# Kernel tuning notes

Hardware: AMD Instinct MI355X
Metric: run time of the kernel (lower is better)

The kernel has to match this reference:

```python
import jax, jax.numpy as jnp
import numpy as np

NUM_HEADS = 8
SR_RATIO = 2
LN_EPS = 1e-5


def setup_inputs() -> dict:
    key = jax.random.key(0)
    ks = jax.random.split(key, 8)
    B, N, C = 8, 4096, 512
    s = 0.02  # weight init scale to keep logits sane
    return {
        "x": jax.random.normal(ks[0], (B, N, C), jnp.float32),
        "q_w": jax.random.normal(ks[1], (C, C), jnp.float32) * s,
        "q_b": jnp.zeros((C,), jnp.float32),
        "kv_w": jax.random.normal(ks[2], (2 * C, C), jnp.float32) * s,
        "kv_b": jnp.zeros((2 * C,), jnp.float32),
        "sr_w": jax.random.normal(ks[3], (C, C, SR_RATIO, SR_RATIO), jnp.float32) * s,
        "sr_b": jnp.zeros((C,), jnp.float32),
        "ln_g": jnp.ones((C,), jnp.float32),
        "ln_b": jnp.zeros((C,), jnp.float32),
        "proj_w": jax.random.normal(ks[4], (C, C), jnp.float32) * s,
        "proj_b": jnp.zeros((C,), jnp.float32),
        "H": 64,
        "W": 64,
    }


def _layernorm(x, g, b):
    mu = jnp.mean(x, axis=-1, keepdims=True)
    var = jnp.var(x, axis=-1, keepdims=True)
    return (x - mu) * jax.lax.rsqrt(var + LN_EPS) * g + b


def reference(x, q_w, q_b, kv_w, kv_b, sr_w, sr_b, ln_g, ln_b, proj_w, proj_b, H, W):
    B, N, C = x.shape
    h = NUM_HEADS
    d = C // h
    scale = d ** (-0.5)

    # q: [B, h, N, d]
    q = (x @ q_w.T + q_b).reshape(B, N, h, d).transpose(0, 2, 1, 3)

    # spatial reduction: Conv2d(C, C, k=SR, stride=SR) on [B, C, H, W]
    x_img = x.transpose(0, 2, 1).reshape(B, C, H, W)
    x_sr = jax.lax.conv_general_dilated(
        x_img, sr_w,
        window_strides=(SR_RATIO, SR_RATIO), padding="VALID",
        dimension_numbers=("NCHW", "OIHW", "NCHW"),
    ) + sr_b[None, :, None, None]
    N2 = (H // SR_RATIO) * (W // SR_RATIO)
    x_sr = x_sr.reshape(B, C, N2).transpose(0, 2, 1)  # [B, N2, C]
    x_sr = _layernorm(x_sr, ln_g, ln_b)

    # kv: [2, B, h, N2, d]
    kv = (x_sr @ kv_w.T + kv_b).reshape(B, N2, 2, h, d).transpose(2, 0, 3, 1, 4)
    k, v = kv[0], kv[1]

    attn = jax.nn.softmax(jnp.einsum("bhnd,bhmd->bhnm", q, k) * scale, axis=-1)
    out = jnp.einsum("bhnm,bhmd->bhnd", attn, v)  # [B, h, N, d]
    out = out.transpose(0, 2, 1, 3).reshape(B, N, C)
    return out @ proj_w.T + proj_b
```

## Files before the change

kernel.cpp:

```cpp
#include <hip/hip_runtime.h>
#include <hip/hip_bf16.h>

typedef __hip_bfloat16 bf16;
typedef __bf16 bf16x8 __attribute__((ext_vector_type(8)));
typedef float f32x16 __attribute__((ext_vector_type(16)));
typedef unsigned int u32;
typedef unsigned int u32x2 __attribute__((ext_vector_type(2)));

typedef const __attribute__((address_space(1))) void GV;
typedef __attribute__((address_space(3))) void LV;

#define TM 128
#define TN 128
#define TK 64

static __device__ __forceinline__ float fexp2(float x) {
#if __has_builtin(__builtin_amdgcn_exp2f)
    return __builtin_amdgcn_exp2f(x);
#else
    return exp2f(x);
#endif
}

__global__ void prep_k(const float* __restrict__ x, const float* __restrict__ qw,
                       const float* __restrict__ kvw, const float* __restrict__ pjw,
                       const float* __restrict__ srw,
                       bf16* __restrict__ xb, bf16* __restrict__ qwb,
                       bf16* __restrict__ kvwb, bf16* __restrict__ pjwb,
                       bf16* __restrict__ srwb) {
    const int bid = blockIdx.x;
    const int tid = threadIdx.x;
    if (bid < 17408) {
        const float* src;
        bf16* dst;
        int i;
        if (bid < 16384)      { src = x;   dst = xb;   i = bid * 256 + tid; }
        else if (bid < 16640) { src = qw;  dst = qwb;  i = (bid - 16384) * 256 + tid; }
        else if (bid < 17152) { src = kvw; dst = kvwb; i = (bid - 16640) * 256 + tid; }
        else                  { src = pjw; dst = pjwb; i = (bid - 17152) * 256 + tid; }
        float4 a = reinterpret_cast<const float4*>(src)[i];
        bf16* d = dst + (size_t)i * 4;
        d[0] = __float2bfloat16(a.x);
        d[1] = __float2bfloat16(a.y);
        d[2] = __float2bfloat16(a.z);
        d[3] = __float2bfloat16(a.w);
    } else {
        int idx = (bid - 17408) * 256 + tid;
        int co = idx >> 11;
        int t  = idx & 2047;
        int p  = t >> 9;
        int ci = t & 511;
        srwb[idx] = __float2bfloat16(srw[(size_t)co * 2048 + ci * 4 + p]);
    }
}

template<int KIND>
__device__ __forceinline__ void gemm_body(int bid, bf16* ldsA, bf16* ldsB,
                                          const bf16* __restrict__ A, const bf16* __restrict__ Bw,
                                          const float* __restrict__ bias,
                                          bf16* __restrict__ outB, bf16* __restrict__ outB2,
                                          float* __restrict__ outF, int N, int K) {
    const int tid = threadIdx.x;
    const int lane = tid & 63;
    const int wave = tid >> 6;
    const int ntn = N / TN;
    const int row0 = (bid / ntn) * TM;
    const int col0 = (bid % ntn) * TN;
    const int wm = wave >> 1, wn = wave & 1;
    const int l31 = lane & 31;
    const int hi8 = lane >> 5;
    const int NK = K / TK;

    f32x16 acc[2][2];
#pragma unroll
    for (int i = 0; i < 2; ++i)
#pragma unroll
        for (int j = 0; j < 2; ++j) acc[i][j] = f32x16{};

    auto stage = [&](int ks, int buf) {
        const int k0 = ks * TK;
        bf16* la = ldsA + buf * (TM * TK);
        bf16* lb = ldsB + buf * (TM * TK);
#pragma unroll
        for (int t = 0; t < 4; ++t) {
            int idx = t * 256 + tid;
            int r = idx >> 3;
            int c = ((idx & 7) ^ (r & 7)) * 8;
            const bf16* src;
            if (KIND == 1) {
                int rr = row0 + r;
                int k = k0 + c;
                int p = k >> 9, ci = k & 511;
                int b = rr >> 10, ii = (rr >> 5) & 31, jj = rr & 31;
                int n_in = (2 * ii + (p >> 1)) * 64 + 2 * jj + (p & 1);
                src = A + ((size_t)(b * 4096 + n_in)) * 512 + ci;
            } else {
                src = A + (size_t)(row0 + r) * K + k0 + c;
            }
            __builtin_amdgcn_global_load_lds((GV*)src, (LV*)&la[idx * 8], 16, 0, 0);
        }
#pragma unroll
        for (int t = 0; t < 4; ++t) {
            int idx = t * 256 + tid;
            int r = idx >> 3;
            int c = ((idx & 7) ^ (r & 7)) * 8;
            const bf16* src = Bw + (size_t)(col0 + r) * K + k0 + c;
            __builtin_amdgcn_global_load_lds((GV*)src, (LV*)&lb[idx * 8], 16, 0, 0);
        }
    };

    stage(0, 0);
    stage(1, 1);

    int cur = 0;
    for (int ks = 0; ks < NK; ++ks) {
        if (ks < NK - 1) asm volatile("s_waitcnt vmcnt(8)" ::: "memory");
        else             asm volatile("s_waitcnt vmcnt(0)" ::: "memory");
        __builtin_amdgcn_s_barrier();

        const bf16* la = ldsA + cur * (TM * TK);
        const bf16* lb = ldsB + cur * (TM * TK);
#pragma unroll
        for (int kk = 0; kk < 4; ++kk) {
            bf16x8 af[2], bfr[2];
#pragma unroll
            for (int m = 0; m < 2; ++m) {
                int row = wm * 64 + m * 32 + l31;
                int chunk = (kk * 2 + hi8) ^ (row & 7);
                af[m] = *reinterpret_cast<const bf16x8*>(&la[row * 64 + chunk * 8]);
            }
#pragma unroll
            for (int n = 0; n < 2; ++n) {
                int row = wn * 64 + n * 32 + l31;
                int chunk = (kk * 2 + hi8) ^ (row & 7);
                bfr[n] = *reinterpret_cast<const bf16x8*>(&lb[row * 64 + chunk * 8]);
            }
#pragma unroll
            for (int m = 0; m < 2; ++m)
#pragma unroll
                for (int n = 0; n < 2; ++n)
                    acc[m][n] = __builtin_amdgcn_mfma_f32_32x32x16_bf16(af[m], bfr[n], acc[m][n], 0, 0, 0);
        }

        __builtin_amdgcn_s_barrier();
        if (ks + 2 < NK) stage(ks + 2, cur);
        cur ^= 1;
    }

#pragma unroll
    for (int m = 0; m < 2; ++m) {
#pragma unroll
        for (int n = 0; n < 2; ++n) {
#pragma unroll
            for (int r = 0; r < 16; ++r) {
                int grow = row0 + wm * 64 + m * 32 + (r & 3) + 8 * (r >> 2) + 4 * (lane >> 5);
                int gcol = col0 + wn * 64 + n * 32 + l31;
                float v = acc[m][n][r] + bias[gcol];
                if (KIND == 0) {
                    int b = grow >> 12, nn = grow & 4095;
                    int h = gcol >> 6, dd = gcol & 63;
                    outB[(((size_t)(b * 8 + h)) * 4096 + nn) * 64 + dd] =
                        __float2bfloat16(v * 0.18033688011112042f);
                } else if (KIND == 1) {
                    outF[(size_t)grow * 512 + gcol] = v;
                } else if (KIND == 2) {
                    int b = grow >> 10, mm = grow & 1023;
                    if (gcol < 512) {
                        int h = gcol >> 6, dd = gcol & 63;
                        outB[(((size_t)(b * 8 + h)) * 1024 + mm) * 64 + dd] = __float2bfloat16(v);
                    } else {
                        int c2 = gcol - 512;
                        int h = c2 >> 6, dd = c2 & 63;
                        outB2[(((size_t)(b * 8 + h)) * 64 + dd) * 1024 + mm] = __float2bfloat16(v);
                    }
                } else {
                    outF[(size_t)grow * 512 + gcol] = v;
                }
            }
        }
    }
}

__launch_bounds__(256, 2)
__global__ void gemm01_k(const bf16* __restrict__ xb, const bf16* __restrict__ qw,
                         const bf16* __restrict__ srw, const float* __restrict__ q_b,
                         const float* __restrict__ sr_b,
                         bf16* __restrict__ q_out, float* __restrict__ xsr_out) {
    __shared__ __align__(16) bf16 ldsA[2][TM * TK];
    __shared__ __align__(16) bf16 ldsB[2][TM * TK];
    if (blockIdx.x < 256)
        gemm_body<1>(blockIdx.x, &ldsA[0][0], &ldsB[0][0], xb, srw, sr_b,
                     nullptr, nullptr, xsr_out, 512, 2048);
    else
        gemm_body<0>(blockIdx.x - 256, &ldsA[0][0], &ldsB[0][0], xb, qw, q_b,
                     q_out, nullptr, nullptr, 512, 512);
}

__launch_bounds__(256, 2)
__global__ void gemm2_k(const bf16* __restrict__ A, const bf16* __restrict__ Bw,
                        const float* __restrict__ bias,
                        bf16* __restrict__ kout, bf16* __restrict__ vtout) {
    __shared__ __align__(16) bf16 ldsA[2][TM * TK];
    __shared__ __align__(16) bf16 ldsB[2][TM * TK];
    gemm_body<2>(blockIdx.x, &ldsA[0][0], &ldsB[0][0], A, Bw, bias, kout, vtout, nullptr, 1024, 512);
}

__launch_bounds__(256, 2)
__global__ void gemm3_k(const bf16* __restrict__ A, const bf16* __restrict__ Bw,
                        const float* __restrict__ bias, float* __restrict__ outF) {
    __shared__ __align__(16) bf16 ldsA[2][TM * TK];
    __shared__ __align__(16) bf16 ldsB[2][TM * TK];
    gemm_body<3>(blockIdx.x, &ldsA[0][0], &ldsB[0][0], A, Bw, bias, nullptr, nullptr, outF, 512, 512);
}

__global__ void ln_k(const float* __restrict__ xsr, const float* __restrict__ g,
                     const float* __restrict__ bta, bf16* __restrict__ out) {
    const int row = blockIdx.x;
    const int tid = threadIdx.x;
    const float* xr = xsr + (size_t)row * 512;
    float2 v = *reinterpret_cast<const float2*>(xr + tid * 2);
    float s = v.x + v.y;
    float sq = v.x * v.x + v.y * v.y;
#pragma unroll
    for (int m = 1; m < 64; m <<= 1) {
        s += __shfl_xor(s, m, 64);
        sq += __shfl_xor(sq, m, 64);
    }
    __shared__ float rs[4], rq[4];
    int wave = tid >> 6, lane = tid & 63;
    if (lane == 0) { rs[wave] = s; rq[wave] = sq; }
    __syncthreads();
    s = rs[0] + rs[1] + rs[2] + rs[3];
    sq = rq[0] + rq[1] + rq[2] + rq[3];
    float mu = s * (1.f / 512.f);
    float var = sq * (1.f / 512.f) - mu * mu;
    float rstd = rsqrtf(var + 1e-5f);
    bf16* orow = out + (size_t)row * 512;
    orow[tid * 2]     = __float2bfloat16((v.x - mu) * rstd * g[tid * 2] + bta[tid * 2]);
    orow[tid * 2 + 1] = __float2bfloat16((v.y - mu) * rstd * g[tid * 2 + 1] + bta[tid * 2 + 1]);
}

__launch_bounds__(256, 4)
__global__ void attn_k(const bf16* __restrict__ Q, const bf16* __restrict__ Kb,
                       const bf16* __restrict__ Vt, bf16* __restrict__ Out) {
    const int p = blockIdx.x;
    const int bh = (p & 7) * 8 + (p >> 8);
    const int qb = (p >> 3) & 31;
    const int b = bh >> 3, h = bh & 7;
    const int tid = threadIdx.x, lane = tid & 63, wave = tid >> 6;
    const int q0 = qb * 128 + wave * 32;
    const int l31 = lane & 31;
    const int klo8 = (lane >> 5) * 8;

    const bf16* Qp = Q + ((size_t)bh * 4096 + q0) * 64;
    const bf16* Kp = Kb + (size_t)bh * 1024 * 64;
    const bf16* Vp = Vt + (size_t)bh * 64 * 1024;

    __shared__ __align__(16) char smem[32768];

    bf16x8 qf[4];
#pragma unroll
    for (int c = 0; c < 4; ++c)
        qf[c] = *reinterpret_cast<const bf16x8*>(Qp + (size_t)l31 * 64 + c * 16 + klo8);

    f32x16 accO[2];
    accO[0] = f32x16{};
    accO[1] = f32x16{};
    f32x16 accL = f32x16{};
    const f32x16 z16 = f32x16{};

    union { u32 u[4]; bf16x8 v; } onesu;
    onesu.u[0] = 0x3F803F80u; onesu.u[1] = 0x3F803F80u;
    onesu.u[2] = 0x3F803F80u; onesu.u[3] = 0x3F803F80u;
    const bf16x8 ones8 = onesu.v;

    const int l2 = lane >> 1;
    const int lh8 = (lane & 1) * 8;
    const int w16 = wave * 16;

    const char* rb = smem + l31 * 32 + (lane >> 5) * 16;

#define STAGE_TILE(KT, BASE)                                                              \
    do {                                                                                  \
        char* _b = (BASE);                                                                \
        __builtin_amdgcn_global_load_lds((GV*)(Kp + (size_t)((KT) + l2) * 64 + w16 + lh8),\
                                         (LV*)(_b + wave * 2048), 16, 0, 0);              \
        __builtin_amdgcn_global_load_lds((GV*)(Kp + (size_t)((KT) + 32 + l2) * 64 + w16 + lh8),\
                                         (LV*)(_b + wave * 2048 + 1024), 16, 0, 0);       \
        __builtin_amdgcn_global_load_lds((GV*)(Vp + (size_t)l2 * 1024 + (KT) + w16 + lh8),\
                                         (LV*)(_b + 8192 + wave * 2048), 16, 0, 0);       \
        __builtin_amdgcn_global_load_lds((GV*)(Vp + (size_t)(32 + l2) * 1024 + (KT) + w16 + lh8),\
                                         (LV*)(_b + 8192 + wave * 2048 + 1024), 16, 0, 0);\
    } while (0)

    STAGE_TILE(0, smem);
    STAGE_TILE(64, smem + 16384);

    int cur = 0;
    for (int t = 0; t < 16; ++t) {
        if (t < 15) asm volatile("s_waitcnt vmcnt(4)" ::: "memory");
        else        asm volatile("s_waitcnt vmcnt(0)" ::: "memory");
        __builtin_amdgcn_s_barrier();

        const char* rc = rb + cur * 16384;

        bf16x8 kf0[4], kf1[4];
#pragma unroll
        for (int c = 0; c < 4; ++c) {
            kf0[c] = *reinterpret_cast<const bf16x8*>(rc + c * 2048);
            kf1[c] = *reinterpret_cast<const bf16x8*>(rc + c * 2048 + 1024);
        }
        f32x16 sA = __builtin_amdgcn_mfma_f32_32x32x16_bf16(kf0[0], qf[0], z16, 0, 0, 0);
        f32x16 sB = __builtin_amdgcn_mfma_f32_32x32x16_bf16(kf1[0], qf[0], z16, 0, 0, 0);
#pragma unroll
        for (int c = 1; c < 4; ++c) {
            sA = __builtin_amdgcn_mfma_f32_32x32x16_bf16(kf0[c], qf[c], sA, 0, 0, 0);
            sB = __builtin_amdgcn_mfma_f32_32x32x16_bf16(kf1[c], qf[c], sB, 0, 0, 0);
        }

        float pA[16], pB[16];
#pragma unroll
        for (int r = 0; r < 16; ++r) pA[r] = fexp2(sA[r]);
#pragma unroll
        for (int r = 0; r < 16; ++r) pB[r] = fexp2(sB[r]);

        u32 wA[8], wB[8];
#pragma unroll
        for (int k = 0; k < 8; ++k) {
            union { __hip_bfloat162 h2; u32 u; } cv;
            cv.h2 = __float22bfloat162_rn(float2{pA[2 * k], pA[2 * k + 1]});
            wA[k] = cv.u;
            union { __hip_bfloat162 h2; u32 u; } cw;
            cw.h2 = __float22bfloat162_rn(float2{pB[2 * k], pB[2 * k + 1]});
            wB[k] = cw.u;
        }
        union { u32 u[4]; bf16x8 v; } fr[4];
        {
            u32x2 e0 = __builtin_amdgcn_permlane32_swap(wA[0], wA[2], false, false);
            u32x2 e1 = __builtin_amdgcn_permlane32_swap(wA[1], wA[3], false, false);
            fr[0].u[0] = e0[0]; fr[0].u[1] = e1[0]; fr[0].u[2] = e0[1]; fr[0].u[3] = e1[1];
            u32x2 e2 = __builtin_amdgcn_permlane32_swap(wA[4], wA[6], false, false);
            u32x2 e3 = __builtin_amdgcn_permlane32_swap(wA[5], wA[7], false, false);
            fr[1].u[0] = e2[0]; fr[1].u[1] = e3[0]; fr[1].u[2] = e2[1]; fr[1].u[3] = e3[1];
            u32x2 e4 = __builtin_amdgcn_permlane32_swap(wB[0], wB[2], false, false);
            u32x2 e5 = __builtin_amdgcn_permlane32_swap(wB[1], wB[3], false, false);
            fr[2].u[0] = e4[0]; fr[2].u[1] = e5[0]; fr[2].u[2] = e4[1]; fr[2].u[3] = e5[1];
            u32x2 e6 = __builtin_amdgcn_permlane32_swap(wB[4], wB[6], false, false);
            u32x2 e7 = __builtin_amdgcn_permlane32_swap(wB[5], wB[7], false, false);
            fr[3].u[0] = e6[0]; fr[3].u[1] = e7[0]; fr[3].u[2] = e6[1]; fr[3].u[3] = e7[1];
        }

        __builtin_amdgcn_s_setprio(1);
#pragma unroll
        for (int dd = 0; dd < 2; ++dd) {
#pragma unroll
            for (int kk = 0; kk < 4; ++kk) {
                bf16x8 vv = *reinterpret_cast<const bf16x8*>(rc + 8192 + kk * 2048 + dd * 1024);
                accO[dd] = __builtin_amdgcn_mfma_f32_32x32x16_bf16(vv, fr[kk].v, accO[dd], 0, 0, 0);
            }
        }
#pragma unroll
        for (int kk = 0; kk < 4; ++kk)
            accL = __builtin_amdgcn_mfma_f32_32x32x16_bf16(ones8, fr[kk].v, accL, 0, 0, 0);
        __builtin_amdgcn_s_setprio(0);

        __builtin_amdgcn_s_barrier();
        if (t + 2 < 16) STAGE_TILE((t + 2) * 64, smem + cur * 16384);
        cur ^= 1;
    }

    __syncthreads();

    typedef bf16 (*ObufT)[32][72];
    ObufT obuf = (ObufT)smem;
    float inv = 1.f / accL[0];
#pragma unroll
    for (int dd = 0; dd < 2; ++dd)
#pragma unroll
        for (int r = 0; r < 16; r += 2) {
            int d = dd * 32 + (r & 3) + 8 * (r >> 2) + 4 * (lane >> 5);
            union { __hip_bfloat162 h2; u32 u; } cv;
            cv.h2 = __float22bfloat162_rn(float2{accO[dd][r] * inv, accO[dd][r + 1] * inv});
            *reinterpret_cast<u32*>(&obuf[wave][l31][d]) = cv.u;
        }
    __syncthreads();
    {
        int qr = lane >> 1, hf = lane & 1;
        const bf16* orow = &obuf[wave][qr][hf * 32];
        bf16* gout = Out + ((size_t)b * 4096 + q0 + qr) * 512 + h * 64 + hf * 32;
#pragma unroll
        for (int j = 0; j < 4; ++j) {
            bf16x8 t2 = *reinterpret_cast<const bf16x8*>(orow + j * 8);
            *reinterpret_cast<bf16x8*>(gout + j * 8) = t2;
        }
    }
#undef STAGE_TILE
}

extern "C" void kernel_launch(void* const* d_in, const int* in_sizes, int n_in,
                              void* d_out, int out_size, void* d_ws, size_t ws_size,
                              hipStream_t stream) {
    const float* x      = (const float*)d_in[0];
    const float* q_w    = (const float*)d_in[1];
    const float* q_b    = (const float*)d_in[2];
    const float* kv_w   = (const float*)d_in[3];
    const float* kv_b   = (const float*)d_in[4];
    const float* sr_w   = (const float*)d_in[5];
    const float* sr_b   = (const float*)d_in[6];
    const float* ln_g   = (const float*)d_in[7];
    const float* ln_b   = (const float*)d_in[8];
    const float* proj_w = (const float*)d_in[9];
    const float* proj_b = (const float*)d_in[10];

    char* w = (char*)d_ws;
    bf16* x_bf   = (bf16*)w; w += (size_t)8 * 4096 * 512 * 2;
    bf16* q_bf   = (bf16*)w; w += (size_t)8 * 4096 * 512 * 2;
    bf16* qw_bf  = (bf16*)w; w += (size_t)512 * 512 * 2;
    bf16* kvw_bf = (bf16*)w; w += (size_t)1024 * 512 * 2;
    bf16* srw_bf = (bf16*)w; w += (size_t)512 * 2048 * 2;
    bf16* pjw_bf = (bf16*)w; w += (size_t)512 * 512 * 2;
    float* xsr_f = (float*)w; w += (size_t)8 * 1024 * 512 * 4;
    bf16* xsrb   = (bf16*)w; w += (size_t)8 * 1024 * 512 * 2;
    bf16* k_bf   = (bf16*)w; w += (size_t)8 * 8 * 1024 * 64 * 2;
    bf16* vt_bf  = (bf16*)w; w += (size_t)8 * 8 * 1024 * 64 * 2;
    bf16* ao_bf  = (bf16*)w; w += (size_t)8 * 4096 * 512 * 2;

    prep_k<<<dim3(21504), dim3(256), 0, stream>>>(x, q_w, kv_w, proj_w, sr_w,
                                                  x_bf, qw_bf, kvw_bf, pjw_bf, srw_bf);

    gemm01_k<<<dim3(1280), dim3(256), 0, stream>>>(x_bf, qw_bf, srw_bf, q_b, sr_b, q_bf, xsr_f);
    ln_k<<<dim3(8192), dim3(256), 0, stream>>>(xsr_f, ln_g, ln_b, xsrb);
    gemm2_k<<<dim3(512), dim3(256), 0, stream>>>(xsrb, kvw_bf, kv_b, k_bf, vt_bf);
    attn_k<<<dim3(2048), dim3(256), 0, stream>>>(q_bf, k_bf, vt_bf, ao_bf);
    gemm3_k<<<dim3(1024), dim3(256), 0, stream>>>(ao_bf, pjw_bf, proj_b, (float*)d_out);
}
```

Measured before the change: 235.3 us.

## Replace double-buffered GEMM LDS pipeline with single buffer for higher occupancy

Measured after the change: 234.9 us. Within noise of the previous version (-0.1%).

```diff
diff --git a/kernel.cpp b/kernel.cpp
--- a/kernel.cpp
+++ b/kernel.cpp
@@ -77,10 +77,8 @@
 #pragma unroll
         for (int j = 0; j < 2; ++j) acc[i][j] = f32x16{};
 
-    auto stage = [&](int ks, int buf) {
+    for (int ks = 0; ks < NK; ++ks) {
         const int k0 = ks * TK;
-        bf16* la = ldsA + buf * (TM * TK);
-        bf16* lb = ldsB + buf * (TM * TK);
 #pragma unroll
         for (int t = 0; t < 4; ++t) {
             int idx = t * 256 + tid;
@@ -97,7 +95,7 @@
             } else {
                 src = A + (size_t)(row0 + r) * K + k0 + c;
             }
-            __builtin_amdgcn_global_load_lds((GV*)src, (LV*)&la[idx * 8], 16, 0, 0);
+            __builtin_amdgcn_global_load_lds((GV*)src, (LV*)&ldsA[idx * 8], 16, 0, 0);
         }
 #pragma unroll
         for (int t = 0; t < 4; ++t) {
@@ -105,21 +103,10 @@
             int r = idx >> 3;
             int c = ((idx & 7) ^ (r & 7)) * 8;
             const bf16* src = Bw + (size_t)(col0 + r) * K + k0 + c;
-            __builtin_amdgcn_global_load_lds((GV*)src, (LV*)&lb[idx * 8], 16, 0, 0);
-        }
-    };
-
-    stage(0, 0);
-    stage(1, 1);
-
-    int cur = 0;
-    for (int ks = 0; ks < NK; ++ks) {
-        if (ks < NK - 1) asm volatile("s_waitcnt vmcnt(8)" ::: "memory");
-        else             asm volatile("s_waitcnt vmcnt(0)" ::: "memory");
-        __builtin_amdgcn_s_barrier();
-
-        const bf16* la = ldsA + cur * (TM * TK);
-        const bf16* lb = ldsB + cur * (TM * TK);
+            __builtin_amdgcn_global_load_lds((GV*)src, (LV*)&ldsB[idx * 8], 16, 0, 0);
+        }
+        __syncthreads();
+
 #pragma unroll
         for (int kk = 0; kk < 4; ++kk) {
             bf16x8 af[2], bfr[2];
@@ -127,13 +114,13 @@
             for (int m = 0; m < 2; ++m) {
                 int row = wm * 64 + m * 32 + l31;
                 int chunk = (kk * 2 + hi8) ^ (row & 7);
-                af[m] = *reinterpret_cast<const bf16x8*>(&la[row * 64 + chunk * 8]);
+                af[m] = *reinterpret_cast<const bf16x8*>(&ldsA[row * 64 + chunk * 8]);
             }
 #pragma unroll
             for (int n = 0; n < 2; ++n) {
                 int row = wn * 64 + n * 32 + l31;
                 int chunk = (kk * 2 + hi8) ^ (row & 7);
-                bfr[n] = *reinterpret_cast<const bf16x8*>(&lb[row * 64 + chunk * 8]);
+                bfr[n] = *reinterpret_cast<const bf16x8*>(&ldsB[row * 64 + chunk * 8]);
             }
 #pragma unroll
             for (int m = 0; m < 2; ++m)
@@ -141,10 +128,7 @@
                 for (int n = 0; n < 2; ++n)
                     acc[m][n] = __builtin_amdgcn_mfma_f32_32x32x16_bf16(af[m], bfr[n], acc[m][n], 0, 0, 0);
         }
-
-        __builtin_amdgcn_s_barrier();
-        if (ks + 2 < NK) stage(ks + 2, cur);
-        cur ^= 1;
+        __syncthreads();
     }
 
 #pragma unroll
@@ -181,36 +165,36 @@
     }
 }
 
-__launch_bounds__(256, 2)
+__launch_bounds__(256, 3)
 __global__ void gemm01_k(const bf16* __restrict__ xb, const bf16* __restrict__ qw,
                          const bf16* __restrict__ srw, const float* __restrict__ q_b,
                          const float* __restrict__ sr_b,
                          bf16* __restrict__ q_out, float* __restrict__ xsr_out) {
-    __shared__ __align__(16) bf16 ldsA[2][TM * TK];
-    __shared__ __align__(16) bf16 ldsB[2][TM * TK];
+    __shared__ __align__(16) bf16 ldsA[TM * TK];
+    __shared__ __align__(16) bf16 ldsB[TM * TK];
     if (blockIdx.x < 256)
-        gemm_body<1>(blockIdx.x, &ldsA[0][0], &ldsB[0][0], xb, srw, sr_b,
+        gemm_body<1>(blockIdx.x, ldsA, ldsB, xb, srw, sr_b,
                      nullptr, nullptr, xsr_out, 512, 2048);
     else
-        gemm_body<0>(blockIdx.x - 256, &ldsA[0][0], &ldsB[0][0], xb, qw, q_b,
+        gemm_body<0>(blockIdx.x - 256, ldsA, ldsB, xb, qw, q_b,
                      q_out, nullptr, nullptr, 512, 512);
 }
 
-__launch_bounds__(256, 2)
+__launch_bounds__(256, 3)
 __global__ void gemm2_k(const bf16* __restrict__ A, const bf16* __restrict__ Bw,
                         const float* __restrict__ bias,
                         bf16* __restrict__ kout, bf16* __restrict__ vtout) {
-    __shared__ __align__(16) bf16 ldsA[2][TM * TK];
-    __shared__ __align__(16) bf16 ldsB[2][TM * TK];
-    gemm_body<2>(blockIdx.x, &ldsA[0][0], &ldsB[0][0], A, Bw, bias, kout, vtout, nullptr, 1024, 512);
-}
-
-__launch_bounds__(256, 2)
+    __shared__ __align__(16) bf16 ldsA[TM * TK];
+    __shared__ __align__(16) bf16 ldsB[TM * TK];
+    gemm_body<2>(blockIdx.x, ldsA, ldsB, A, Bw, bias, kout, vtout, nullptr, 1024, 512);
+}
+
+__launch_bounds__(256, 3)
 __global__ void gemm3_k(const bf16* __restrict__ A, const bf16* __restrict__ Bw,
                         const float* __restrict__ bias, float* __restrict__ outF) {
-    __shared__ __align__(16) bf16 ldsA[2][TM * TK];
-    __shared__ __align__(16) bf16 ldsB[2][TM * TK];
-    gemm_body<3>(blockIdx.x, &ldsA[0][0], &ldsB[0][0], A, Bw, bias, nullptr, nullptr, outF, 512, 512);
+    __shared__ __align__(16) bf16 ldsA[TM * TK];
+    __shared__ __align__(16) bf16 ldsB[TM * TK];
+    gemm_body<3>(blockIdx.x, ldsA, ldsB, A, Bw, bias, nullptr, nullptr, outF, 512, 512);
 }
 
 __global__ void ln_k(const float* __restrict__ xsr, const float* __restrict__ g,
```
